# Optimization experiments

Measured on AMD Instinct MI355X. Metric: run time of the kernel, lower is better.

The kernel has to match this reference:

```python
import jax, jax.numpy as jnp
import numpy as np

D_MODEL = 512
STATE_DIM = 6
D_STATE = 16
D_CONV = 4
EXPAND = 2
D_INNER = EXPAND * D_MODEL            # 1024
DT_RANK = -(-D_MODEL // 16)           # ceil(d_model/16) = 32


def setup_inputs() -> dict:
    key = jax.random.key(0)
    ks = jax.random.split(key, 12)
    s = 0.02
    return {
        "features": jax.random.normal(ks[0], (32, 2048, D_MODEL), dtype=jnp.float32),
        # Mamba params (mamba_ssm defaults: in/out_proj bias=False, conv+dt_proj bias=True)
        "in_proj_w": jax.random.normal(ks[1], (2 * D_INNER, D_MODEL), dtype=jnp.float32) * s,
        "conv_w": jax.random.normal(ks[2], (D_INNER, D_CONV), dtype=jnp.float32) * s,
        "conv_b": jnp.zeros((D_INNER,), dtype=jnp.float32),
        "x_proj_w": jax.random.normal(ks[3], (DT_RANK + 2 * D_STATE, D_INNER), dtype=jnp.float32) * s,
        "dt_proj_w": jax.random.normal(ks[4], (D_INNER, DT_RANK), dtype=jnp.float32) * s,
        "dt_proj_b": jax.random.normal(ks[5], (D_INNER,), dtype=jnp.float32) * s,
        "A_log": jnp.log(jnp.broadcast_to(jnp.arange(1, D_STATE + 1, dtype=jnp.float32), (D_INNER, D_STATE))),
        "D": jnp.ones((D_INNER,), dtype=jnp.float32),
        "out_proj_w": jax.random.normal(ks[6], (D_MODEL, D_INNER), dtype=jnp.float32) * s,
        # trailing fc head: d_model -> state_dim**2
        "fc_w": jax.random.normal(ks[7], (STATE_DIM * STATE_DIM, D_MODEL), dtype=jnp.float32) * s,
        "fc_b": jnp.zeros((STATE_DIM * STATE_DIM,), dtype=jnp.float32),
    }


def reference(features, in_proj_w, conv_w, conv_b, x_proj_w, dt_proj_w, dt_proj_b,
              A_log, D, out_proj_w, fc_w, fc_b):
    # Original loops Mamba over timesteps with seq_len=1 slices -> each timestep is
    # independent. Flatten (batch, seq) into one token axis and vectorize.
    B_, T, dm = features.shape
    f = features.reshape(B_ * T, dm)                      # (N, d_model)

    xz = f @ in_proj_w.T                                  # (N, 2*d_inner)
    x, z = jnp.split(xz, 2, axis=-1)
    # causal depthwise conv on a length-1 sequence: only the last tap contributes
    x = jax.nn.silu(x * conv_w[:, -1] + conv_b)           # (N, d_inner)

    x_dbl = x @ x_proj_w.T                                # (N, dt_rank + 2*d_state)
    dt = x_dbl[:, :DT_RANK]
    Bm = x_dbl[:, DT_RANK:DT_RANK + D_STATE]              # (N, d_state)
    Cm = x_dbl[:, DT_RANK + D_STATE:]                     # (N, d_state)
    delta = jax.nn.softplus(dt @ dt_proj_w.T + dt_proj_b) # (N, d_inner)

    # single-step selective scan with h0 = 0:
    #   h = exp(delta*A)*0 + delta*B*x ;  y = sum_s C_s h_s + D*x
    # (A_log therefore never affects the output for seq_len=1 calls)
    bc = jnp.sum(Bm * Cm, axis=-1, keepdims=True)         # (N, 1)
    y = delta * x * bc + D * x                            # (N, d_inner)
    y = y * jax.nn.silu(z)

    out = y @ out_proj_w.T                                # (N, d_model)
    A_flat = out @ fc_w.T + fc_b                          # (N, state_dim**2)
    return A_flat.reshape(B_, T, STATE_DIM, STATE_DIM)
```

## Files before the change

### kernel.cpp

```cpp
#include <hip/hip_runtime.h>

typedef unsigned short u16;
typedef unsigned int u32;
typedef __attribute__((ext_vector_type(8))) short bf16x8;
typedef __attribute__((ext_vector_type(4))) float f32x4;

#define NTOK 65536
#define DM 512
#define DI 1024

__device__ __forceinline__ float bf2f(u16 u){ u32 x=((u32)u)<<16; float f; __builtin_memcpy(&f,&x,4); return f; }
__device__ __forceinline__ u16 f2bf(float f){ u32 u; __builtin_memcpy(&u,&f,4); u += 0x7fffu + ((u>>16)&1u); return (u16)(u>>16); }
__device__ __forceinline__ float siluf(float x){ return x/(1.f+__expf(-x)); }
__device__ __forceinline__ float softplus_fast(float x){
  float l = __logf(1.f + __expf(x));
  return (x > 20.f) ? x : l;
}

__device__ __forceinline__ void gload_lds16(const void* g, void* l){
  __builtin_amdgcn_global_load_lds((const __attribute__((address_space(1))) u32*)g,
                                   (__attribute__((address_space(3))) u32*)l, 16, 0, 0);
}

__global__ void k_sentinel(float* out){ out[0] = 1.2345e6f; }

__global__ void k_cast_bf16(const float* __restrict__ in, u16* __restrict__ out, int n){
  int i = (blockIdx.x*256 + threadIdx.x)*4;
  if (i >= n) return;
  float4 v = *(const float4*)(in + i);
  ushort4 o; o.x=f2bf(v.x); o.y=f2bf(v.y); o.z=f2bf(v.z); o.w=f2bf(v.w);
  *(ushort4*)(out + i) = o;
}

__global__ void k_cast_weights(const float* __restrict__ ipw_f, const float* __restrict__ xpw_f,
                               const float* __restrict__ dpw_f,
                               u16* __restrict__ ipw, u16* __restrict__ xpw, u16* __restrict__ dpw){
  int b = blockIdx.x;
  const float* src; u16* dst; int base;
  if (b < 1024){ src=ipw_f; dst=ipw; base = b*1024; }
  else if (b < 1088){ src=xpw_f; dst=xpw; base = (b-1024)*1024; }
  else { src=dpw_f; dst=dpw; base = (b-1088)*1024; }
  int i = base + threadIdx.x*4;
  float4 v = *(const float4*)(src + i);
  ushort4 o; o.x=f2bf(v.x); o.y=f2bf(v.y); o.z=f2bf(v.z); o.w=f2bf(v.w);
  *(ushort4*)(dst + i) = o;
}

__global__ void k_make_wa(const float* __restrict__ fcw, const float* __restrict__ opw,
                          u16* __restrict__ wa){
  int j = blockIdx.x*256 + threadIdx.x;
  int i = blockIdx.y;
  float s = 0.f;
  if (i < 36){
    const float* fr = fcw + i*DM;
    #pragma unroll 8
    for (int k=0;k<DM;++k) s += fr[k]*opw[(size_t)k*DI + j];
  }
  wa[(size_t)i*DI + j] = f2bf(s);
}

__global__ __launch_bounds__(256) void k_gemm_xz(
  const u16* __restrict__ A, const u16* __restrict__ B,
  const float* __restrict__ convw, const float* __restrict__ convb,
  u16* __restrict__ xp, u16* __restrict__ zs)
{
  __shared__ u16 smem[32768];
  u16* SA = smem;
  u16* SB = smem + 16384;
  const int tid=threadIdx.x, wv=tid>>6, ln=tid&63;
  const int l15=ln&15, l4=ln>>4, h=l15&7;
  const int l = blockIdx.y*16 + blockIdx.x;
  const int xcd = l & 7, q = l >> 3;
  const int cb = q & 15;
  const int g  = (q >> 4)*8 + xcd;
  const int c0g = cb*128, r0 = g*128;
  const int wm=wv>>1, wn=wv&1;
  const int sr=ln>>3, scs=((ln&7)^sr)*8;
  const int chk0=(l4^h)*8, chk1=((l4+4)^h)*8;
  const int rA=(wm*64+l15)*64, rB=(wn*64+l15)*64;
  f32x4 acc[4][4]={};

  auto STAGE=[&](int buf, int k0){
    u16* Ad = SA + buf*8192;
    u16* Bd = SB + buf*8192;
    #pragma unroll
    for (int it=0;it<4;++it){
      int c=wv*4+it;
      gload_lds16(A + (size_t)(r0 + c*8 + sr)*DM + k0 + scs, Ad + c*512);
    }
    #pragma unroll
    for (int it=0;it<4;++it){
      int c=wv*4+it;
      gload_lds16(B + (size_t)(c0g + c*8 + sr)*DM + k0 + scs, Bd + c*512);
    }
  };

  STAGE(0, 0);
  __syncthreads();
  __builtin_amdgcn_sched_barrier(0);
  int cur = 0;
  #pragma clang loop unroll(disable)
  for (int t=0;t<8;++t){
    if (t < 7) STAGE(cur^1, (t+1)*64);
    const u16* Ac = SA + cur*8192;
    const u16* Bc = SB + cur*8192;
    #pragma unroll
    for (int kk=0;kk<2;++kk){
      const int ch = kk ? chk1 : chk0;
      bf16x8 af[4], bfr[4];
      #pragma unroll
      for (int m=0;m<4;++m) af[m]=*(const bf16x8*)(Ac + rA + m*1024 + ch);
      #pragma unroll
      for (int n=0;n<4;++n) bfr[n]=*(const bf16x8*)(Bc + rB + n*1024 + ch);
      #pragma unroll
      for (int m=0;m<4;++m)
        #pragma unroll
        for (int n=0;n<4;++n)
          acc[m][n]=__builtin_amdgcn_mfma_f32_16x16x32_bf16(af[m],bfr[n],acc[m][n],0,0,0);
    }
    __syncthreads();
    __builtin_amdgcn_sched_barrier(0);
    cur ^= 1;
  }

  const bool isx = (c0g < DI);
  const int cc0 = isx ? c0g : c0g - DI;
  u16* ep = smem;
  #pragma unroll
  for (int n=0;n<4;++n){
    int tcol = wn*64 + n*16 + l15;
    int gcol = c0g + tcol;
    float cw = isx ? convw[gcol*4+3] : 0.f;
    float cb2= isx ? convb[gcol]     : 0.f;
    #pragma unroll
    for (int m=0;m<4;++m){
      int trow = wm*64 + m*16 + l4*4;
      #pragma unroll
      for (int r=0;r<4;++r){
        float v = acc[m][n][r];
        float o = isx ? siluf(v*cw + cb2) : siluf(v);
        ep[(trow+r)*160 + tcol] = f2bf(o);
      }
    }
  }
  __syncthreads();
  int rrow = tid>>1, half = tid&1;
  const u16* srcp = ep + rrow*160 + half*64;
  u16* dst = (isx ? xp : zs) + (size_t)(r0+rrow)*DI + cc0 + half*64;
  #pragma unroll
  for (int j=0;j<8;++j)
    *(int4*)(dst + j*8) = *(const int4*)(srcp + j*8);
}

__global__ __launch_bounds__(256) void k_tail(
  const u16* __restrict__ xp, const u16* __restrict__ xpw,
  const u16* __restrict__ dpw,
  const float* __restrict__ dpb, const float* __restrict__ Dv,
  const u16* __restrict__ zs, const u16* __restrict__ wa,
  const float* __restrict__ fcb, float* __restrict__ out)
{
  __shared__ u16 smem[29952];
  u16*   As  = smem;
  float* bcs = (float*)(smem + 4096);
  u16*   S   = smem + 4352;
  const int tid=threadIdx.x, wv=tid>>6, ln=tid&63;
  const int l15=ln&15, l4=ln>>4, h=l15&7;
  const int r0=blockIdx.x*128;
  const int wm=wv>>1, wn=wv&1;
  const int sr=ln>>3, scs=((ln&7)^sr)*8;
  const int chk0=(l4^h)*8, chk1=((l4+4)^h)*8;
  const int rA=(wm*64+l15)*64, rB=(wn*32+l15)*64;
  const int sr2=ln>>2, sc2=(ln&3)*8;

  {
    f32x4 acc[4][2]={};
    auto STAGE=[&](int buf, int k0){
      u16* Ad = S + buf*8192;
      u16* Bd = S + 16384 + buf*4096;
      #pragma unroll
      for (int it=0;it<4;++it){
        int c=wv*4+it;
        gload_lds16(xp + (size_t)(r0 + c*8 + sr)*DI + k0 + scs, Ad + c*512);
      }
      #pragma unroll
      for (int it=0;it<2;++it){
        int c=wv*2+it;
        gload_lds16(xpw + (size_t)(c*8 + sr)*DI + k0 + scs, Bd + c*512);
      }
    };
    STAGE(0, 0);
    __syncthreads();
    __builtin_amdgcn_sched_barrier(0);
    int cur = 0;
    #pragma clang loop unroll(disable)
    for (int t=0;t<16;++t){
      if (t < 15) STAGE(cur^1, (t+1)*64);
      const u16* Ac = S + cur*8192;
      const u16* Bc = S + 16384 + cur*4096;
      #pragma unroll
      for (int kk=0;kk<2;++kk){
        const int ch = kk ? chk1 : chk0;
        bf16x8 af[4], bfr[2];
        #pragma unroll
        for (int m=0;m<4;++m) af[m]=*(const bf16x8*)(Ac + rA + m*1024 + ch);
        #pragma unroll
        for (int n=0;n<2;++n) bfr[n]=*(const bf16x8*)(Bc + rB + n*1024 + ch);
        #pragma unroll
        for (int m=0;m<4;++m)
          #pragma unroll
          for (int n=0;n<2;++n)
            acc[m][n]=__builtin_amdgcn_mfma_f32_16x16x32_bf16(af[m],bfr[n],acc[m][n],0,0,0);
      }
      __syncthreads();
      __builtin_amdgcn_sched_barrier(0);
      cur ^= 1;
    }
    float* W = (float*)S;
    #pragma unroll
    for (int n=0;n<2;++n){
      int j = wn*32 + n*16 + l15;
      #pragma unroll
      for (int m=0;m<4;++m){
        int trow = wm*64 + m*16 + l4*4;
        #pragma unroll
        for (int r=0;r<4;++r)
          W[(trow+r)*68 + j] = acc[m][n][r];
      }
    }
    __syncthreads();
    const int row = tid>>1, half = tid&1;
    const float* wr = W + row*68;
    if (half==0){
      #pragma unroll
      for (int qv=0;qv<4;++qv){
        bf16x8 o;
        #pragma unroll
        for (int e=0;e<8;++e) o[e] = (short)f2bf(wr[qv*8+e]);
        *(bf16x8*)(As + row*32 + qv*8) = o;
      }
    } else {
      float s=0.f;
      #pragma unroll
      for (int e=0;e<16;++e) s += wr[32+e]*wr[48+e];
      bcs[row] = s;
    }
    {
      u16* Bs0 = S + 17408;
      #pragma unroll
      for (int it=0;it<2;++it){
        int c=wv*2+it;
        gload_lds16(dpw + (size_t)(c*16 + sr2)*32 + sc2, Bs0 + c*512);
      }
    }
    __syncthreads();
  }

  u16* Y   = S;
  u16* BsB = S + 17408;
  bf16x8 af[4];
  #pragma unroll
  for (int m=0;m<4;++m) af[m]=*(const bf16x8*)(As + (wm*64+m*16+l15)*32 + l4*8);

  f32x4 oacc[2][4]={};
  const int yrow = tid>>1, yhalf = tid&1;
  int cur = 0;

  #pragma clang loop unroll(disable)
  for (int ch=0; ch<8; ++ch){
    f32x4 dacc[4][4]={};
    bf16x8 bfr[4];
    #pragma unroll
    for (int n=0;n<4;++n) bfr[n]=*(const bf16x8*)(BsB + cur*4096 + (wn*64+n*16+l15)*32 + l4*8);
    #pragma unroll
    for (int m=0;m<4;++m)
      #pragma unroll
      for (int n=0;n<4;++n)
        dacc[m][n]=__builtin_amdgcn_mfma_f32_16x16x32_bf16(af[m],bfr[n],dacc[m][n],0,0,0);
    if (ch<7){
      #pragma unroll
      for (int it=0;it<2;++it){
        int c=wv*2+it;
        gload_lds16(dpw + (size_t)((ch+1)*128 + c*16 + sr2)*32 + sc2, BsB + (cur^1)*4096 + c*512);
      }
    }
    #pragma unroll
    for (int n=0;n<4;++n){
      int tcol = wn*64 + n*16 + l15;
      int j = ch*128 + tcol;
      float dpbj = dpb[j], Dj = Dv[j];
      #pragma unroll
      for (int m=0;m<4;++m){
        int trow = wm*64 + m*16 + l4*4;
        #pragma unroll
        for (int r=0;r<4;++r){
          float delta = softplus_fast(dacc[m][n][r] + dpbj);
          float w = delta*bcs[trow + r] + Dj;
          Y[(trow+r)*136 + tcol] = f2bf(w);
        }
      }
    }
    __syncthreads();
    {
      u16* wp = Y + yrow*136 + yhalf*64;
      const size_t gbase = (size_t)(r0 + yrow)*DI + ch*128 + yhalf*64;
      const u16* xpp = xp + gbase;
      const u16* zp  = zs + gbase;
      #pragma unroll
      for (int qq=0;qq<8;++qq){
        bf16x8 wv8 = *(const bf16x8*)(wp + qq*8);
        bf16x8 xv  = *(const bf16x8*)(xpp + qq*8);
        bf16x8 zv  = *(const bf16x8*)(zp + qq*8);
        bf16x8 ov;
        #pragma unroll
        for (int e=0;e<8;++e){
          float y = bf2f((u16)wv8[e]) * bf2f((u16)xv[e]) * bf2f((u16)zv[e]);
          ov[e] = (short)f2bf(y);
        }
        *(bf16x8*)(wp + qq*8) = ov;
      }
    }
    __syncthreads();
    #pragma unroll
    for (int kk=0;kk<4;++kk){
      bf16x8 af2[2], bf2r[4];
      #pragma unroll
      for (int m=0;m<2;++m)
        af2[m]=*(const bf16x8*)(Y + (wv*32 + m*16 + l15)*136 + kk*32 + l4*8);
      #pragma unroll
      for (int n=0;n<4;++n)
        bf2r[n]=*(const bf16x8*)(wa + (size_t)(n*16 + l15)*DI + ch*128 + kk*32 + l4*8);
      #pragma unroll
      for (int m=0;m<2;++m)
        #pragma unroll
        for (int n=0;n<4;++n)
          oacc[m][n]=__builtin_amdgcn_mfma_f32_16x16x32_bf16(af2[m],bf2r[n],oacc[m][n],0,0,0);
    }
    __syncthreads();
    __builtin_amdgcn_sched_barrier(0);
    cur ^= 1;
  }

  #pragma unroll
  for (int n=0;n<4;++n){
    int j = n*16 + l15;
    if (j < 36){
      float fj = fcb[j];
      #pragma unroll
      for (int m=0;m<2;++m){
        #pragma unroll
        for (int r=0;r<4;++r){
          int t = r0 + wv*32 + m*16 + l4*4 + r;
          out[(size_t)t*36 + j] = oacc[m][n][r] + fj;
        }
      }
    }
  }
}

extern "C" void kernel_launch(void* const* d_in, const int* in_sizes, int n_in,
                              void* d_out, int out_size, void* d_ws, size_t ws_size,
                              hipStream_t stream){
  const float* f      = (const float*)d_in[0];
  const float* inpw   = (const float*)d_in[1];
  const float* convw  = (const float*)d_in[2];
  const float* convb  = (const float*)d_in[3];
  const float* xprojw = (const float*)d_in[4];
  const float* dtpw   = (const float*)d_in[5];
  const float* dtpb   = (const float*)d_in[6];
  const float* Dv     = (const float*)d_in[8];
  const float* opw    = (const float*)d_in[9];
  const float* fcw    = (const float*)d_in[10];
  const float* fcb    = (const float*)d_in[11];
  float* out = (float*)d_out;

  char* ws = (char*)d_ws;
  size_t off = 0;
  auto alloc = [&](size_t sz)->void*{ void* p = ws + off; off += (sz + 255) & ~(size_t)255; return p; };
  u16*   fbf = (u16*)  alloc((size_t)NTOK*DM*2);
  u16*   xp  = (u16*)  alloc((size_t)NTOK*DI*2);
  u16*   zy  = (u16*)  alloc((size_t)NTOK*DI*2);
  u16*   ipw = (u16*)  alloc((size_t)2048*512*2);
  u16*   xpw = (u16*)  alloc((size_t)64*1024*2);
  u16*   dpw = (u16*)  alloc((size_t)1024*32*2);
  u16*   wa  = (u16*)  alloc((size_t)64*1024*2);
  if (off > ws_size){ k_sentinel<<<1,1,0,stream>>>(out); return; }

  k_cast_bf16<<<dim3((NTOK*DM/4)/256),256,0,stream>>>(f, fbf, NTOK*DM);
  k_cast_weights<<<dim3(1120),256,0,stream>>>(inpw, xprojw, dtpw, ipw, xpw, dpw);
  k_make_wa<<<dim3(4,64),256,0,stream>>>(fcw, opw, wa);

  k_gemm_xz<<<dim3(16,512),256,0,stream>>>(fbf, ipw, convw, convb, xp, zy);
  k_tail<<<dim3(512),256,0,stream>>>(xp, xpw, dpw, dtpb, Dv, zy, wa, fcb, out);
}
```

Before: 467.5 us.

## Load A fragments directly from global into registers, stage only B in LDS

The xz GEMM now skips staging the A tile through LDS. Each wave loads its own A fragments straight from global memory into registers and double-buffers them across k-steps, while B stays double-buffered in LDS. The aim is to cut LDS footprint and traffic, which could allow higher occupancy, and to remove the LDS reads for A. In exchange, A rows are read from global by both wn-halves of the block (duplicate traffic), the loads may coalesce less well, and register pressure rises from the afn/afc buffers.

```diff
diff --git a/kernel.cpp b/kernel.cpp
--- a/kernel.cpp
+++ b/kernel.cpp
@@ -64,9 +64,7 @@
   const float* __restrict__ convw, const float* __restrict__ convb,
   u16* __restrict__ xp, u16* __restrict__ zs)
 {
-  __shared__ u16 smem[32768];
-  u16* SA = smem;
-  u16* SB = smem + 16384;
+  __shared__ u16 smem[20480];
   const int tid=threadIdx.x, wv=tid>>6, ln=tid&63;
   const int l15=ln&15, l4=ln>>4, h=l15&7;
   const int l = blockIdx.y*16 + blockIdx.x;
@@ -77,17 +75,11 @@
   const int wm=wv>>1, wn=wv&1;
   const int sr=ln>>3, scs=((ln&7)^sr)*8;
   const int chk0=(l4^h)*8, chk1=((l4+4)^h)*8;
-  const int rA=(wm*64+l15)*64, rB=(wn*64+l15)*64;
+  const int rB=(wn*64+l15)*64;
   f32x4 acc[4][4]={};
 
-  auto STAGE=[&](int buf, int k0){
-    u16* Ad = SA + buf*8192;
-    u16* Bd = SB + buf*8192;
-    #pragma unroll
-    for (int it=0;it<4;++it){
-      int c=wv*4+it;
-      gload_lds16(A + (size_t)(r0 + c*8 + sr)*DM + k0 + scs, Ad + c*512);
-    }
+  auto STAGE_B=[&](int buf, int k0){
+    u16* Bd = smem + buf*8192;
     #pragma unroll
     for (int it=0;it<4;++it){
       int c=wv*4+it;
@@ -95,31 +87,47 @@
     }
   };
 
-  STAGE(0, 0);
+  const u16* Ap[4];
+  #pragma unroll
+  for (int m=0;m<4;++m) Ap[m] = A + (size_t)(r0 + wm*64 + m*16 + l15)*DM + l4*8;
+
+  bf16x8 afc[4][2], afn[4][2];
+  #pragma unroll
+  for (int m=0;m<4;++m){
+    afc[m][0] = *(const bf16x8*)(Ap[m]);
+    afc[m][1] = *(const bf16x8*)(Ap[m] + 32);
+  }
+  STAGE_B(0, 0);
   __syncthreads();
   __builtin_amdgcn_sched_barrier(0);
   int cur = 0;
   #pragma clang loop unroll(disable)
   for (int t=0;t<8;++t){
-    if (t < 7) STAGE(cur^1, (t+1)*64);
-    const u16* Ac = SA + cur*8192;
-    const u16* Bc = SB + cur*8192;
+    if (t < 7){
+      STAGE_B(cur^1, (t+1)*64);
+      #pragma unroll
+      for (int m=0;m<4;++m){
+        afn[m][0] = *(const bf16x8*)(Ap[m] + (t+1)*64);
+        afn[m][1] = *(const bf16x8*)(Ap[m] + (t+1)*64 + 32);
+      }
+    }
+    const u16* Bc = smem + cur*8192;
     #pragma unroll
     for (int kk=0;kk<2;++kk){
       const int ch = kk ? chk1 : chk0;
-      bf16x8 af[4], bfr[4];
-      #pragma unroll
-      for (int m=0;m<4;++m) af[m]=*(const bf16x8*)(Ac + rA + m*1024 + ch);
+      bf16x8 bfr[4];
       #pragma unroll
       for (int n=0;n<4;++n) bfr[n]=*(const bf16x8*)(Bc + rB + n*1024 + ch);
       #pragma unroll
       for (int m=0;m<4;++m)
         #pragma unroll
         for (int n=0;n<4;++n)
-          acc[m][n]=__builtin_amdgcn_mfma_f32_16x16x32_bf16(af[m],bfr[n],acc[m][n],0,0,0);
+          acc[m][n]=__builtin_amdgcn_mfma_f32_16x16x32_bf16(afc[m][kk],bfr[n],acc[m][n],0,0,0);
     }
     __syncthreads();
     __builtin_amdgcn_sched_barrier(0);
+    #pragma unroll
+    for (int m=0;m<4;++m){ afc[m][0]=afn[m][0]; afc[m][1]=afn[m][1]; }
     cur ^= 1;
   }
 
```

Result: slower. 583.2 us (+24.8%).

## Rewrite in_proj GEMM as 256x256 tiles with 8 waves and interleaved staging

Applied to the files above, without the earlier changes.

The xz GEMM moves from 128x128 tiles on 256 threads to 256x256 tiles on 512 threads (8 waves, 2x4 layout) with 128KB of LDS. Global-to-LDS loads for the next k-tile are split into half-tile chunks and interleaved with MFMA phases, using explicit vmcnt waits, s_barrier and setprio to overlap memory with compute. The larger tile is meant to raise arithmetic intensity and cut redundant reloads of A and B. In exchange occupancy drops to one block per CU and the epilogue writes out in two column halves.

```diff
diff --git a/kernel.cpp b/kernel.cpp
--- a/kernel.cpp
+++ b/kernel.cpp
@@ -59,97 +59,129 @@
   wa[(size_t)i*DI + j] = f2bf(s);
 }
 
-__global__ __launch_bounds__(256) void k_gemm_xz(
+__global__ __launch_bounds__(512,1) void k_gemm_xz(
   const u16* __restrict__ A, const u16* __restrict__ B,
   const float* __restrict__ convw, const float* __restrict__ convb,
   u16* __restrict__ xp, u16* __restrict__ zs)
 {
-  __shared__ u16 smem[32768];
-  u16* SA = smem;
-  u16* SB = smem + 16384;
+  __shared__ u16 smem[65536];
   const int tid=threadIdx.x, wv=tid>>6, ln=tid&63;
-  const int l15=ln&15, l4=ln>>4, h=l15&7;
-  const int l = blockIdx.y*16 + blockIdx.x;
-  const int xcd = l & 7, q = l >> 3;
-  const int cb = q & 15;
-  const int g  = (q >> 4)*8 + xcd;
-  const int c0g = cb*128, r0 = g*128;
-  const int wm=wv>>1, wn=wv&1;
-  const int sr=ln>>3, scs=((ln&7)^sr)*8;
-  const int chk0=(l4^h)*8, chk1=((l4+4)^h)*8;
-  const int rA=(wm*64+l15)*64, rB=(wn*64+l15)*64;
-  f32x4 acc[4][4]={};
-
-  auto STAGE=[&](int buf, int k0){
-    u16* Ad = SA + buf*8192;
-    u16* Bd = SB + buf*8192;
-    #pragma unroll
-    for (int it=0;it<4;++it){
-      int c=wv*4+it;
-      gload_lds16(A + (size_t)(r0 + c*8 + sr)*DM + k0 + scs, Ad + c*512);
-    }
-    #pragma unroll
-    for (int it=0;it<4;++it){
-      int c=wv*4+it;
-      gload_lds16(B + (size_t)(c0g + c*8 + sr)*DM + k0 + scs, Bd + c*512);
-    }
+  const int l15=ln&15, l4=ln>>4;
+  const int l=blockIdx.x, xcd=l&7, q0=l>>3;
+  const int cb=q0&7, g=(q0>>3)*8+xcd;
+  const size_t r0=(size_t)g*256; const int c0=cb*256;
+  const int wm=wv>>2, wn=wv&3;
+  const int bnh=wn>>1, bc0=(wn&1)*64;
+  f32x4 acc[8][4]={};
+
+  const u16* baseA[2]; const u16* baseB[2]; int dsto[2];
+  #pragma unroll
+  for(int j=0;j<2;++j){
+    int c=j*8+wv, kc=c>>1, rh=c&1;
+    baseA[j]=A + (r0 + rh*64 + ln)*DM + kc*8;
+    baseB[j]=B + (size_t)(c0 + rh*64 + ln)*DM + kc*8;
+    dsto[j]=kc*1024 + rh*512;
+  }
+  auto STAGE_A=[&](int d,int kt,int h){
+    #pragma unroll
+    for(int j=0;j<2;++j)
+      gload_lds16(baseA[j] + (size_t)h*128*DM + kt*64, smem + d*32768 + h*8192 + dsto[j]);
   };
-
-  STAGE(0, 0);
+  auto STAGE_B=[&](int d,int kt,int h){
+    #pragma unroll
+    for(int j=0;j<2;++j)
+      gload_lds16(baseB[j] + (size_t)h*128*DM + kt*64, smem + d*32768 + 16384 + h*8192 + dsto[j]);
+  };
+  bf16x8 bq[4][2];
+  auto LDB=[&](int d){
+    #pragma unroll
+    for(int n=0;n<4;++n)
+      #pragma unroll
+      for(int kk=0;kk<2;++kk)
+        bq[n][kk]=*(const bf16x8*)(smem + d*32768 + 16384 + bnh*8192 + (kk*4+l4)*1024 + (bc0+n*16+l15)*8);
+  };
+  auto MM=[&](int d,int m0){
+    bf16x8 af[2][2];
+    #pragma unroll
+    for(int mm=0;mm<2;++mm)
+      #pragma unroll
+      for(int kk=0;kk<2;++kk)
+        af[mm][kk]=*(const bf16x8*)(smem + d*32768 + wm*8192 + (kk*4+l4)*1024 + ((m0+mm)*16+l15)*8);
+    __builtin_amdgcn_s_barrier();
+    asm volatile("s_waitcnt lgkmcnt(0)" ::: "memory");
+    __builtin_amdgcn_sched_barrier(0);
+    __builtin_amdgcn_s_setprio(1);
+    #pragma unroll
+    for(int mm=0;mm<2;++mm)
+      #pragma unroll
+      for(int kk=0;kk<2;++kk)
+        #pragma unroll
+        for(int n=0;n<4;++n)
+          acc[m0+mm][n]=__builtin_amdgcn_mfma_f32_16x16x32_bf16(af[mm][kk],bq[n][kk],acc[m0+mm][n],0,0,0);
+    __builtin_amdgcn_s_setprio(0);
+  };
+  auto ENDP=[&](){ __builtin_amdgcn_s_barrier(); __builtin_amdgcn_sched_barrier(0); };
+
+  STAGE_A(0,0,0); STAGE_A(0,0,1); STAGE_B(0,0,0); STAGE_B(0,0,1);
+  STAGE_B(1,1,0); STAGE_B(1,1,1);
+  asm volatile("s_waitcnt vmcnt(4)" ::: "memory");
+  __builtin_amdgcn_s_barrier();
+  __builtin_amdgcn_sched_barrier(0);
+
+  #pragma clang loop unroll(disable)
+  for(int i=0;i<4;++i){
+    const bool st=(i<3);
+    LDB(0);
+    STAGE_A(1,2*i+1,0); MM(0,0); ENDP();
+    STAGE_A(1,2*i+1,1); MM(0,2); ENDP();
+    if(st) STAGE_B(0,2*i+2,0); MM(0,4); ENDP();
+    if(st) STAGE_B(0,2*i+2,1); MM(0,6);
+    if(st) asm volatile("s_waitcnt vmcnt(4)" ::: "memory");
+    else   asm volatile("s_waitcnt vmcnt(0)" ::: "memory");
+    ENDP();
+    LDB(1);
+    if(st) STAGE_A(0,2*i+2,0); MM(1,0); ENDP();
+    if(st) STAGE_A(0,2*i+2,1); MM(1,2); ENDP();
+    if(st) STAGE_B(1,2*i+3,0); MM(1,4); ENDP();
+    if(st) STAGE_B(1,2*i+3,1); MM(1,6);
+    if(st) asm volatile("s_waitcnt vmcnt(4)" ::: "memory");
+    ENDP();
+  }
   __syncthreads();
-  __builtin_amdgcn_sched_barrier(0);
-  int cur = 0;
-  #pragma clang loop unroll(disable)
-  for (int t=0;t<8;++t){
-    if (t < 7) STAGE(cur^1, (t+1)*64);
-    const u16* Ac = SA + cur*8192;
-    const u16* Bc = SB + cur*8192;
-    #pragma unroll
-    for (int kk=0;kk<2;++kk){
-      const int ch = kk ? chk1 : chk0;
-      bf16x8 af[4], bfr[4];
-      #pragma unroll
-      for (int m=0;m<4;++m) af[m]=*(const bf16x8*)(Ac + rA + m*1024 + ch);
-      #pragma unroll
-      for (int n=0;n<4;++n) bfr[n]=*(const bf16x8*)(Bc + rB + n*1024 + ch);
-      #pragma unroll
-      for (int m=0;m<4;++m)
-        #pragma unroll
-        for (int n=0;n<4;++n)
-          acc[m][n]=__builtin_amdgcn_mfma_f32_16x16x32_bf16(af[m],bfr[n],acc[m][n],0,0,0);
-    }
-    __syncthreads();
-    __builtin_amdgcn_sched_barrier(0);
-    cur ^= 1;
-  }
-
-  const bool isx = (c0g < DI);
-  const int cc0 = isx ? c0g : c0g - DI;
-  u16* ep = smem;
+
+  const bool isx=(c0<DI);
+  const int cc0= isx? c0 : c0-DI;
+  u16* W=smem;
   #pragma unroll
-  for (int n=0;n<4;++n){
-    int tcol = wn*64 + n*16 + l15;
-    int gcol = c0g + tcol;
-    float cw = isx ? convw[gcol*4+3] : 0.f;
-    float cb2= isx ? convb[gcol]     : 0.f;
-    #pragma unroll
-    for (int m=0;m<4;++m){
-      int trow = wm*64 + m*16 + l4*4;
-      #pragma unroll
-      for (int r=0;r<4;++r){
-        float v = acc[m][n][r];
-        float o = isx ? siluf(v*cw + cb2) : siluf(v);
-        ep[(trow+r)*160 + tcol] = f2bf(o);
-      }
-    }
-  }
-  __syncthreads();
-  int rrow = tid>>1, half = tid&1;
-  const u16* srcp = ep + rrow*160 + half*64;
-  u16* dst = (isx ? xp : zs) + (size_t)(r0+rrow)*DI + cc0 + half*64;
-  #pragma unroll
-  for (int j=0;j<8;++j)
-    *(int4*)(dst + j*8) = *(const int4*)(srcp + j*8);
+  for(int ch=0;ch<2;++ch){
+    if((wn>>1)==ch){
+      #pragma unroll
+      for(int n=0;n<4;++n){
+        int tcol=(wn&1)*64+n*16+l15;
+        int gcol=c0+ch*128+tcol;
+        float cw = isx? convw[gcol*4+3]:0.f;
+        float cb2= isx? convb[gcol]   :0.f;
+        #pragma unroll
+        for(int m=0;m<8;++m){
+          int trow=wm*128+m*16+l4*4;
+          #pragma unroll
+          for(int r=0;r<4;++r){
+            float v=acc[m][n][r];
+            float o= isx? siluf(v*cw+cb2):siluf(v);
+            W[(trow+r)*136+tcol]=f2bf(o);
+          }
+        }
+      }
+    }
+    __syncthreads();
+    const int row=tid>>1, half=tid&1;
+    const u16* sp=W+row*136+half*64;
+    u16* dst=(isx?xp:zs)+(r0+row)*DI+cc0+ch*128+half*64;
+    #pragma unroll
+    for(int j2=0;j2<8;++j2)
+      ((int4*)dst)[j2]=((const int4*)sp)[j2];
+    __syncthreads();
+  }
 }
 
 __global__ __launch_bounds__(256) void k_tail(
@@ -389,6 +421,6 @@
   k_cast_weights<<<dim3(1120),256,0,stream>>>(inpw, xprojw, dtpw, ipw, xpw, dpw);
   k_make_wa<<<dim3(4,64),256,0,stream>>>(fcw, opw, wa);
 
-  k_gemm_xz<<<dim3(16,512),256,0,stream>>>(fbf, ipw, convw, convb, xp, zy);
+  k_gemm_xz<<<dim3(2048),512,0,stream>>>(fbf, ipw, convw, convb, xp, zy);
   k_tail<<<dim3(512),256,0,stream>>>(xp, xpw, dpw, dtpb, Dv, zy, wa, fcb, out);
 }
```

New measurement: 561.0 us. +20.0%, slower.

## Load GEMM weight fragments directly from global memory instead of LDS staging

Applied to the files above, without the earlier changes.

Both the in_proj GEMM and the tail kernel now read the B-operand (weight) fragments straight from global memory into registers, so those weights are no longer staged through shared memory. The smaller LDS footprint allows raising occupancy hints (launch_bounds 4 and 3 blocks per CU). The weights are shared across blocks and should hit in L2 or MALL. The risk is added global-load latency inside the MFMA loop, since these loads are not software-pipelined, and uncoalesced 16-byte row-strided accesses.

```diff
diff --git a/kernel.cpp b/kernel.cpp
--- a/kernel.cpp
+++ b/kernel.cpp
@@ -59,14 +59,12 @@
   wa[(size_t)i*DI + j] = f2bf(s);
 }
 
-__global__ __launch_bounds__(256) void k_gemm_xz(
+__global__ __launch_bounds__(256,4) void k_gemm_xz(
   const u16* __restrict__ A, const u16* __restrict__ B,
   const float* __restrict__ convw, const float* __restrict__ convb,
   u16* __restrict__ xp, u16* __restrict__ zs)
 {
-  __shared__ u16 smem[32768];
-  u16* SA = smem;
-  u16* SB = smem + 16384;
+  __shared__ u16 smem[17408];
   const int tid=threadIdx.x, wv=tid>>6, ln=tid&63;
   const int l15=ln&15, l4=ln>>4, h=l15&7;
   const int l = blockIdx.y*16 + blockIdx.x;
@@ -77,23 +75,21 @@
   const int wm=wv>>1, wn=wv&1;
   const int sr=ln>>3, scs=((ln&7)^sr)*8;
   const int chk0=(l4^h)*8, chk1=((l4+4)^h)*8;
-  const int rA=(wm*64+l15)*64, rB=(wn*64+l15)*64;
+  const int rA=(wm*64+l15)*64;
   f32x4 acc[4][4]={};
 
   auto STAGE=[&](int buf, int k0){
-    u16* Ad = SA + buf*8192;
-    u16* Bd = SB + buf*8192;
+    u16* Ad = smem + buf*8192;
     #pragma unroll
     for (int it=0;it<4;++it){
       int c=wv*4+it;
       gload_lds16(A + (size_t)(r0 + c*8 + sr)*DM + k0 + scs, Ad + c*512);
     }
-    #pragma unroll
-    for (int it=0;it<4;++it){
-      int c=wv*4+it;
-      gload_lds16(B + (size_t)(c0g + c*8 + sr)*DM + k0 + scs, Bd + c*512);
-    }
   };
+
+  const u16* Bp[4];
+  #pragma unroll
+  for (int n=0;n<4;++n) Bp[n] = B + (size_t)(c0g + wn*64 + n*16 + l15)*DM + l4*8;
 
   STAGE(0, 0);
   __syncthreads();
@@ -102,16 +98,15 @@
   #pragma clang loop unroll(disable)
   for (int t=0;t<8;++t){
     if (t < 7) STAGE(cur^1, (t+1)*64);
-    const u16* Ac = SA + cur*8192;
-    const u16* Bc = SB + cur*8192;
+    const u16* Ac = smem + cur*8192;
     #pragma unroll
     for (int kk=0;kk<2;++kk){
       const int ch = kk ? chk1 : chk0;
       bf16x8 af[4], bfr[4];
       #pragma unroll
+      for (int n=0;n<4;++n) bfr[n]=*(const bf16x8*)(Bp[n] + t*64 + kk*32);
+      #pragma unroll
       for (int m=0;m<4;++m) af[m]=*(const bf16x8*)(Ac + rA + m*1024 + ch);
-      #pragma unroll
-      for (int n=0;n<4;++n) bfr[n]=*(const bf16x8*)(Bc + rB + n*1024 + ch);
       #pragma unroll
       for (int m=0;m<4;++m)
         #pragma unroll
@@ -139,27 +134,27 @@
       for (int r=0;r<4;++r){
         float v = acc[m][n][r];
         float o = isx ? siluf(v*cw + cb2) : siluf(v);
-        ep[(trow+r)*160 + tcol] = f2bf(o);
+        ep[(trow+r)*136 + tcol] = f2bf(o);
       }
     }
   }
   __syncthreads();
   int rrow = tid>>1, half = tid&1;
-  const u16* srcp = ep + rrow*160 + half*64;
+  const u16* srcp = ep + rrow*136 + half*64;
   u16* dst = (isx ? xp : zs) + (size_t)(r0+rrow)*DI + cc0 + half*64;
   #pragma unroll
   for (int j=0;j<8;++j)
     *(int4*)(dst + j*8) = *(const int4*)(srcp + j*8);
 }
 
-__global__ __launch_bounds__(256) void k_tail(
+__global__ __launch_bounds__(256,3) void k_tail(
   const u16* __restrict__ xp, const u16* __restrict__ xpw,
   const u16* __restrict__ dpw,
   const float* __restrict__ dpb, const float* __restrict__ Dv,
   const u16* __restrict__ zs, const u16* __restrict__ wa,
   const float* __restrict__ fcb, float* __restrict__ out)
 {
-  __shared__ u16 smem[29952];
+  __shared__ u16 smem[21760];
   u16*   As  = smem;
   float* bcs = (float*)(smem + 4096);
   u16*   S   = smem + 4352;
@@ -169,25 +164,22 @@
   const int wm=wv>>1, wn=wv&1;
   const int sr=ln>>3, scs=((ln&7)^sr)*8;
   const int chk0=(l4^h)*8, chk1=((l4+4)^h)*8;
-  const int rA=(wm*64+l15)*64, rB=(wn*32+l15)*64;
-  const int sr2=ln>>2, sc2=(ln&3)*8;
+  const int rA=(wm*64+l15)*64;
 
   {
     f32x4 acc[4][2]={};
     auto STAGE=[&](int buf, int k0){
       u16* Ad = S + buf*8192;
-      u16* Bd = S + 16384 + buf*4096;
       #pragma unroll
       for (int it=0;it<4;++it){
         int c=wv*4+it;
         gload_lds16(xp + (size_t)(r0 + c*8 + sr)*DI + k0 + scs, Ad + c*512);
       }
-      #pragma unroll
-      for (int it=0;it<2;++it){
-        int c=wv*2+it;
-        gload_lds16(xpw + (size_t)(c*8 + sr)*DI + k0 + scs, Bd + c*512);
-      }
     };
+    const u16* Bp[2];
+    #pragma unroll
+    for (int n=0;n<2;++n) Bp[n] = xpw + (size_t)(wn*32 + n*16 + l15)*DI + l4*8;
+
     STAGE(0, 0);
     __syncthreads();
     __builtin_amdgcn_sched_barrier(0);
@@ -196,15 +188,14 @@
     for (int t=0;t<16;++t){
       if (t < 15) STAGE(cur^1, (t+1)*64);
       const u16* Ac = S + cur*8192;
-      const u16* Bc = S + 16384 + cur*4096;
       #pragma unroll
       for (int kk=0;kk<2;++kk){
         const int ch = kk ? chk1 : chk0;
         bf16x8 af[4], bfr[2];
         #pragma unroll
+        for (int n=0;n<2;++n) bfr[n]=*(const bf16x8*)(Bp[n] + t*64 + kk*32);
+        #pragma unroll
         for (int m=0;m<4;++m) af[m]=*(const bf16x8*)(Ac + rA + m*1024 + ch);
-        #pragma unroll
-        for (int n=0;n<2;++n) bfr[n]=*(const bf16x8*)(Bc + rB + n*1024 + ch);
         #pragma unroll
         for (int m=0;m<4;++m)
           #pragma unroll
@@ -244,45 +235,29 @@
       for (int e=0;e<16;++e) s += wr[32+e]*wr[48+e];
       bcs[row] = s;
     }
-    {
-      u16* Bs0 = S + 17408;
-      #pragma unroll
-      for (int it=0;it<2;++it){
-        int c=wv*2+it;
-        gload_lds16(dpw + (size_t)(c*16 + sr2)*32 + sc2, Bs0 + c*512);
-      }
-    }
-    __syncthreads();
-  }
-
-  u16* Y   = S;
-  u16* BsB = S + 17408;
+    __syncthreads();
+  }
+
+  u16* Y = S;
   bf16x8 af[4];
   #pragma unroll
   for (int m=0;m<4;++m) af[m]=*(const bf16x8*)(As + (wm*64+m*16+l15)*32 + l4*8);
 
   f32x4 oacc[2][4]={};
   const int yrow = tid>>1, yhalf = tid&1;
-  int cur = 0;
 
   #pragma clang loop unroll(disable)
   for (int ch=0; ch<8; ++ch){
     f32x4 dacc[4][4]={};
     bf16x8 bfr[4];
     #pragma unroll
-    for (int n=0;n<4;++n) bfr[n]=*(const bf16x8*)(BsB + cur*4096 + (wn*64+n*16+l15)*32 + l4*8);
+    for (int n=0;n<4;++n)
+      bfr[n]=*(const bf16x8*)(dpw + (size_t)(ch*128 + wn*64 + n*16 + l15)*32 + l4*8);
     #pragma unroll
     for (int m=0;m<4;++m)
       #pragma unroll
       for (int n=0;n<4;++n)
         dacc[m][n]=__builtin_amdgcn_mfma_f32_16x16x32_bf16(af[m],bfr[n],dacc[m][n],0,0,0);
-    if (ch<7){
-      #pragma unroll
-      for (int it=0;it<2;++it){
-        int c=wv*2+it;
-        gload_lds16(dpw + (size_t)((ch+1)*128 + c*16 + sr2)*32 + sc2, BsB + (cur^1)*4096 + c*512);
-      }
-    }
     #pragma unroll
     for (int n=0;n<4;++n){
       int tcol = wn*64 + n*16 + l15;
@@ -337,7 +312,6 @@
     }
     __syncthreads();
     __builtin_amdgcn_sched_barrier(0);
-    cur ^= 1;
   }
 
   #pragma unroll
```

Measured after the change: 544.8 us. 16.6% more time.
